# Kernel tuning notes

Measured on AMD Instinct MI355X. Metric: run time of the kernel, lower is better.

Reference implementation:

```python
import jax, jax.numpy as jnp
import numpy as np

D_MODEL = 2048
N_Q = 32
N_KV = 8  # num_heads // 4
HEAD_DIM = D_MODEL // N_Q  # 64
CTX = 2048


def precompute_rope_freqs(head_dim, max_seq_len):
    theta = 1.0 / (10000.0 ** (jnp.arange(0, head_dim, 2, dtype=jnp.float32) / head_dim))
    positions = jnp.arange(max_seq_len, dtype=jnp.float32)
    return jnp.outer(positions, theta)  # [T, head_dim//2]


def apply_rope(x, freqs):
    # x: [B, T, H, D]; freqs: [T, D//2]
    T = x.shape[1]
    f = freqs[:T][None, :, None, :]  # [1, T, 1, D//2]
    cos, sin = jnp.cos(f), jnp.sin(f)
    D = x.shape[-1]
    x1, x2 = x[..., : D // 2], x[..., D // 2 :]
    return jnp.concatenate([x1 * cos - x2 * sin, x1 * sin + x2 * cos], axis=-1)


def setup_inputs() -> dict:
    key = jax.random.key(0)
    ks = jax.random.split(key, 10)
    s = 0.02
    B, T = 1, CTX
    inp = {
        "x": jax.random.normal(ks[0], (B, T, D_MODEL), dtype=jnp.float32),
        "Wq": jax.random.normal(ks[1], (D_MODEL, N_Q * HEAD_DIM), dtype=jnp.float32) * s,
        "bq": jnp.zeros((N_Q * HEAD_DIM,), dtype=jnp.float32),
        "Wk": jax.random.normal(ks[2], (D_MODEL, N_KV * HEAD_DIM), dtype=jnp.float32) * s,
        "bk": jnp.zeros((N_KV * HEAD_DIM,), dtype=jnp.float32),
        "Wv": jax.random.normal(ks[3], (D_MODEL, N_KV * HEAD_DIM), dtype=jnp.float32) * s,
        "bv": jnp.zeros((N_KV * HEAD_DIM,), dtype=jnp.float32),
        "Wo": jax.random.normal(ks[4], (D_MODEL, D_MODEL), dtype=jnp.float32) * s,
        "bo": jnp.zeros((D_MODEL,), dtype=jnp.float32),
        "freqs": precompute_rope_freqs(HEAD_DIM, CTX),
    }
    return inp


def reference(x, Wq, bq, Wk, bk, Wv, bv, Wo, bo, freqs):
    B, T, C = x.shape
    q = (x @ Wq + bq).reshape(B, T, N_Q, HEAD_DIM)
    k = (x @ Wk + bk).reshape(B, T, N_KV, HEAD_DIM)
    v = (x @ Wv + bv).reshape(B, T, N_KV, HEAD_DIM)
    q = apply_rope(q, freqs)
    k = apply_rope(k, freqs)
    repeat = N_Q // N_KV
    # repeat_interleave along head dim: q head h uses kv head h // repeat
    k = jnp.repeat(k, repeat, axis=2)
    v = jnp.repeat(v, repeat, axis=2)
    # [B, H, T, D]
    q = q.transpose(0, 2, 1, 3)
    k = k.transpose(0, 2, 1, 3)
    v = v.transpose(0, 2, 1, 3)
    scale = 1.0 / jnp.sqrt(jnp.asarray(HEAD_DIM, dtype=x.dtype))
    scores = jnp.einsum("bhtd,bhsd->bhts", q, k) * scale  # [B, H, T, T]
    causal = jnp.tril(jnp.ones((T, T), dtype=bool))
    scores = jnp.where(causal[None, None], scores, jnp.finfo(scores.dtype).min)
    attn = jax.nn.softmax(scores, axis=-1)
    out = jnp.einsum("bhts,bhsd->bhtd", attn, v)  # [B, H, T, D]
    out = out.transpose(0, 2, 1, 3).reshape(B, T, C)
    return out @ Wo + bo
```

## Files before the change

### kernel.cpp

```cpp
#include <hip/hip_runtime.h>
#include <hip/hip_bf16.h>
#include <math.h>

#define T_CTX 2048
#define DM    2048
#define NQ    32
#define NKV   8
#define HD    64
#define QKV_LD 3072

typedef __attribute__((ext_vector_type(8))) short short8;
typedef __attribute__((ext_vector_type(4))) float floatx4;

__device__ __forceinline__ void gload_lds16(const void* g, void* l) {
  __builtin_amdgcn_global_load_lds(
      (const __attribute__((address_space(1))) void*)g,
      (__attribute__((address_space(3))) void*)l, 16, 0, 0);
}

__device__ __forceinline__ void tcast_body(const float* __restrict__ src,
                                           __hip_bfloat16* __restrict__ dst,
                                           int Ncols, int Krows, int bx, int by,
                                           int tid, float (*tile)[66]) {
  const int n0 = bx * 64, k0 = by * 64;
  const int c = tid & 63, r0 = tid >> 6;
#pragma unroll
  for (int s = 0; s < 16; ++s) {
    int r = r0 + 4 * s;
    tile[r][c] = src[(size_t)(k0 + r) * Ncols + n0 + c];
  }
  __syncthreads();
#pragma unroll
  for (int s = 0; s < 16; ++s) {
    int r = r0 + 4 * s;
    dst[(size_t)(n0 + r) * Krows + k0 + c] = __float2bfloat16(tile[c][r]);
  }
}

__global__ __launch_bounds__(256) void prep_kernel(
    const float* __restrict__ x, const float* __restrict__ Wq,
    const float* __restrict__ Wk, const float* __restrict__ Wv,
    const float* __restrict__ Wo, const float* __restrict__ bq,
    const float* __restrict__ bk, const float* __restrict__ bv,
    __hip_bfloat16* __restrict__ xb, __hip_bfloat16* __restrict__ wt,
    __hip_bfloat16* __restrict__ wot, float* __restrict__ bcat) {
  __shared__ float tile[64][66];
  const int bid = blockIdx.x;
  const int tid = threadIdx.x;
  if (bid < 2048) {
    const int i = bid * 256 + tid;
    const float4 a = ((const float4*)x)[2 * i];
    const float4 b = ((const float4*)x)[2 * i + 1];
    union { ushort u[8]; short8 v; } o;
    __hip_bfloat16 h;
    h = __float2bfloat16(a.x); o.u[0] = *(ushort*)&h;
    h = __float2bfloat16(a.y); o.u[1] = *(ushort*)&h;
    h = __float2bfloat16(a.z); o.u[2] = *(ushort*)&h;
    h = __float2bfloat16(a.w); o.u[3] = *(ushort*)&h;
    h = __float2bfloat16(b.x); o.u[4] = *(ushort*)&h;
    h = __float2bfloat16(b.y); o.u[5] = *(ushort*)&h;
    h = __float2bfloat16(b.z); o.u[6] = *(ushort*)&h;
    h = __float2bfloat16(b.w); o.u[7] = *(ushort*)&h;
    ((short8*)xb)[i] = o.v;
  } else if (bid < 3072) {
    const int lid = bid - 2048;
    tcast_body(Wq, wt, 2048, 2048, lid & 31, lid >> 5, tid, tile);
  } else if (bid < 3328) {
    const int lid = bid - 3072;
    tcast_body(Wk, wt + (size_t)2048 * 2048, 512, 2048, lid & 7, lid >> 3, tid, tile);
  } else if (bid < 3584) {
    const int lid = bid - 3328;
    tcast_body(Wv, wt + (size_t)2560 * 2048, 512, 2048, lid & 7, lid >> 3, tid, tile);
  } else if (bid < 4608) {
    const int lid = bid - 3584;
    tcast_body(Wo, wot, 2048, 2048, lid & 31, lid >> 5, tid, tile);
  } else {
    for (int i = tid; i < 3072; i += 256)
      bcat[i] = (i < 2048) ? bq[i] : ((i < 2560) ? bk[i - 2048] : bv[i - 2560]);
  }
}

template <typename OutT>
__global__ __launch_bounds__(256) void gemm_mfma_bt(
    const __hip_bfloat16* __restrict__ A, const __hip_bfloat16* __restrict__ Bt,
    const float* __restrict__ bias, OutT* __restrict__ C, int K, int ldc) {
  __shared__ alignas(16) short As[2][128 * 64];
  __shared__ alignas(16) short Bs[2][128 * 64];
  const int tid = threadIdx.x;
  const int lane = tid & 63;
  const int w = tid >> 6;
  const int wr = w >> 1, wc = w & 1;
  const int bm = blockIdx.y * 128, bn = blockIdx.x * 128;

  floatx4 acc[4][4];
#pragma unroll
  for (int m = 0; m < 4; ++m)
#pragma unroll
    for (int n = 0; n < 4; ++n) acc[m][n] = floatx4{0.f, 0.f, 0.f, 0.f};

  const int frag_kb = (lane >> 4) * 16;
  const int srow8 = lane >> 3;
  const int sbyte = (lane & 7) * 16;

  auto stage = [&](int buf, int k0) {
#pragma unroll
    for (int i = 0; i < 4; ++i) {
      const int r = w * 32 + i * 8 + srow8;
      const int gcb = sbyte ^ ((r & 7) << 4);
      gload_lds16((const char*)(A + (size_t)(bm + r) * K + k0) + gcb,
                  (char*)(As[buf]) + (w * 32 + i * 8) * 128);
      gload_lds16((const char*)(Bt + (size_t)(bn + r) * K + k0) + gcb,
                  (char*)(Bs[buf]) + (w * 32 + i * 8) * 128);
    }
  };

  stage(0, 0);
  __syncthreads();
  int cur = 0;
  for (int k0 = 0; k0 < K; k0 += 64) {
    if (k0 + 64 < K) stage(cur ^ 1, k0 + 64);
#pragma unroll
    for (int h = 0; h < 2; ++h) {
      short8 af[4], bf[4];
      const int kb = h * 64 + frag_kb;
#pragma unroll
      for (int m = 0; m < 4; ++m) {
        const int ar = wr * 64 + m * 16 + (lane & 15);
        af[m] = *(const short8*)((const char*)(As[cur]) + ar * 128 + (kb ^ ((ar & 7) << 4)));
      }
#pragma unroll
      for (int n = 0; n < 4; ++n) {
        const int br = wc * 64 + n * 16 + (lane & 15);
        bf[n] = *(const short8*)((const char*)(Bs[cur]) + br * 128 + (kb ^ ((br & 7) << 4)));
      }
#pragma unroll
      for (int m = 0; m < 4; ++m)
#pragma unroll
        for (int n = 0; n < 4; ++n)
          acc[m][n] = __builtin_amdgcn_mfma_f32_16x16x32_bf16(af[m], bf[n], acc[m][n], 0, 0, 0);
    }
    __syncthreads();
    cur ^= 1;
  }

  const int col_l = lane & 15;
  const int row_l = (lane >> 4) * 4;
#pragma unroll
  for (int n = 0; n < 4; ++n) {
    const int col = bn + wc * 64 + n * 16 + col_l;
    const float bv = bias[col];
#pragma unroll
    for (int m = 0; m < 4; ++m) {
      const int row0 = bm + wr * 64 + m * 16 + row_l;
#pragma unroll
      for (int r2 = 0; r2 < 4; ++r2) {
        const float v = acc[m][n][r2] + bv;
        if constexpr (sizeof(OutT) == 2)
          C[(size_t)(row0 + r2) * ldc + col] = __float2bfloat16(v);
        else
          C[(size_t)(row0 + r2) * ldc + col] = v;
      }
    }
  }
}

__global__ __launch_bounds__(256) void rope_kernel(__hip_bfloat16* __restrict__ qkv,
                                                   const float* __restrict__ freqs) {
  const int idx = blockIdx.x * 256 + threadIdx.x;
  const int i = idx & 31;
  const int h = (idx >> 5) % 40;
  const int t = idx / (40 * 32);
  const int base = (h < 32) ? h * HD : DM + (h - 32) * HD;
  __hip_bfloat16* p = qkv + (size_t)t * QKV_LD + base;
  const float f = freqs[t * 32 + i];
  float s, c;
  sincosf(f, &s, &c);
  const float x1 = __bfloat162float(p[i]);
  const float x2 = __bfloat162float(p[i + 32]);
  float r1 = x1 * c - x2 * s;
  float r2 = x1 * s + x2 * c;
  if (h < 32) { r1 *= 0.125f; r2 *= 0.125f; }
  p[i]      = __float2bfloat16(r1);
  p[i + 32] = __float2bfloat16(r2);
}

__global__ __launch_bounds__(256) void transpose_v_kernel(
    const __hip_bfloat16* __restrict__ qkv, __hip_bfloat16* __restrict__ vt) {
  __shared__ short tile[64][66];
  const int c0 = blockIdx.x * 64;
  const int t0 = blockIdx.y * 64;
  const int c = threadIdx.x & 63;
  const int r0 = threadIdx.x >> 6;
#pragma unroll
  for (int s = 0; s < 16; ++s) {
    int r = r0 + 4 * s;
    tile[r][c] = *(const short*)(qkv + (size_t)(t0 + r) * QKV_LD + DM + NKV * HD + c0 + c);
  }
  __syncthreads();
#pragma unroll
  for (int s = 0; s < 16; ++s) {
    int r = r0 + 4 * s;
    *(short*)(vt + (size_t)(c0 + r) * T_CTX + t0 + c) = tile[c][r];
  }
}

__global__ __launch_bounds__(256) void attn_mfma_kernel(
    const __hip_bfloat16* __restrict__ qkv, const __hip_bfloat16* __restrict__ vtg,
    __hip_bfloat16* __restrict__ O, __hip_bfloat16* __restrict__ Opart,
    float* __restrict__ mlpart) {
  const int bid = blockIdx.x;
  const int hp = bid / 48;
  const int w48 = bid % 48;
  int qb, t0, t1, half;
  bool split;
  if (w48 < 32) {
    qb = 31 - (w48 >> 1);
    half = w48 & 1;
    const int h = (qb + 2) >> 1;
    split = true;
    t0 = half ? h : 0;
    t1 = half ? (qb + 1) : h;
  } else {
    qb = 15 - (w48 - 32);
    half = 0; split = false;
    t0 = 0; t1 = qb + 1;
  }
  const int h0 = hp * 2;
  const int kvh = h0 >> 2;
  const int tid = threadIdx.x;
  const int lane = tid & 63;
  const int w = tid >> 6;
  const int l15 = lane & 15;
  const int lg = lane >> 4;
  const int qbase = qb * 64 + w * 16;

  __shared__ alignas(16) char Ks[64 * 128];
  __shared__ alignas(16) char Vts[64 * 128];
  __shared__ alignas(16) char Ps[4][2][16 * 128];

  short8 qf[2][2];
#pragma unroll
  for (int hh = 0; hh < 2; ++hh)
#pragma unroll
    for (int kh = 0; kh < 2; ++kh)
      qf[hh][kh] = *(const short8*)(qkv + (size_t)(qbase + l15) * QKV_LD +
                                    (h0 + hh) * HD + kh * 32 + lg * 8);

  floatx4 o_acc[2][4];
  float mrow[2][4], lrow[2][4];
#pragma unroll
  for (int hh = 0; hh < 2; ++hh)
#pragma unroll
    for (int n = 0; n < 4; ++n) o_acc[hh][n] = floatx4{0.f, 0.f, 0.f, 0.f};
#pragma unroll
  for (int hh = 0; hh < 2; ++hh)
#pragma unroll
    for (int r = 0; r < 4; ++r) { mrow[hh][r] = -INFINITY; lrow[hh][r] = 0.f; }

  const __hip_bfloat16* Kg = qkv + DM + kvh * HD;
  const int srow8 = lane >> 3;
  const int sbyte = (lane & 7) * 16;

  for (int kt = t0; kt < t1; ++kt) {
    const int s0 = kt * 64;
    __syncthreads();
#pragma unroll
    for (int i = 0; i < 2; ++i) {
      const int r = w * 16 + i * 8 + srow8;
      const int gcb = sbyte ^ ((r & 7) << 4);
      gload_lds16((const char*)(Kg + (size_t)(s0 + r) * QKV_LD) + gcb,
                  Ks + (w * 16 + i * 8) * 128);
      gload_lds16((const char*)(vtg + (size_t)(kvh * 64 + r) * T_CTX + s0) + gcb,
                  Vts + (w * 16 + i * 8) * 128);
    }
    __syncthreads();

    if (s0 > qbase + 15) continue;

    floatx4 sacc[2][4];
#pragma unroll
    for (int hh = 0; hh < 2; ++hh)
#pragma unroll
      for (int n = 0; n < 4; ++n) sacc[hh][n] = floatx4{0.f, 0.f, 0.f, 0.f};
#pragma unroll
    for (int kh = 0; kh < 2; ++kh) {
      short8 bf[4];
#pragma unroll
      for (int n = 0; n < 4; ++n) {
        const int kr = n * 16 + l15;
        bf[n] = *(const short8*)(Ks + kr * 128 + ((kh * 64 + lg * 16) ^ ((kr & 7) << 4)));
      }
#pragma unroll
      for (int hh = 0; hh < 2; ++hh)
#pragma unroll
        for (int n = 0; n < 4; ++n)
          sacc[hh][n] = __builtin_amdgcn_mfma_f32_16x16x32_bf16(qf[hh][kh], bf[n], sacc[hh][n], 0, 0, 0);
    }
    if (s0 + 63 > qbase) {
#pragma unroll
      for (int n = 0; n < 4; ++n)
#pragma unroll
        for (int r = 0; r < 4; ++r)
          if (s0 + n * 16 + l15 > qbase + lg * 4 + r) {
            sacc[0][n][r] = -INFINITY;
            sacc[1][n][r] = -INFINITY;
          }
    }
#pragma unroll
    for (int hh = 0; hh < 2; ++hh) {
#pragma unroll
      for (int r = 0; r < 4; ++r) {
        float t = fmaxf(fmaxf(sacc[hh][0][r], sacc[hh][1][r]),
                        fmaxf(sacc[hh][2][r], sacc[hh][3][r]));
        t = fmaxf(t, __shfl_xor(t, 1));
        t = fmaxf(t, __shfl_xor(t, 2));
        t = fmaxf(t, __shfl_xor(t, 4));
        t = fmaxf(t, __shfl_xor(t, 8));
        float mn = mrow[hh][r];
        if (t > mn + 8.f) {
          const float corr = __expf(mn - t);
          lrow[hh][r] *= corr;
#pragma unroll
          for (int n = 0; n < 4; ++n) o_acc[hh][n][r] *= corr;
          mn = t;
          mrow[hh][r] = t;
        }
        float pv[4];
        float ls = 0.f;
#pragma unroll
        for (int n = 0; n < 4; ++n) {
          pv[n] = __expf(sacc[hh][n][r] - mn);
          ls += pv[n];
        }
        ls += __shfl_xor(ls, 1);
        ls += __shfl_xor(ls, 2);
        ls += __shfl_xor(ls, 4);
        ls += __shfl_xor(ls, 8);
        lrow[hh][r] += ls;
        const int prow = lg * 4 + r;
#pragma unroll
        for (int n = 0; n < 4; ++n)
          *(__hip_bfloat16*)(Ps[w][hh] + prow * 128 +
                             (((n * 16 + l15) * 2) ^ ((prow & 7) << 4))) =
              __float2bfloat16(pv[n]);
      }
    }
#pragma unroll
    for (int kh = 0; kh < 2; ++kh) {
      short8 vf[4];
#pragma unroll
      for (int n = 0; n < 4; ++n) {
        const int vr = n * 16 + l15;
        vf[n] = *(const short8*)(Vts + vr * 128 + ((kh * 64 + lg * 16) ^ ((vr & 7) << 4)));
      }
#pragma unroll
      for (int hh = 0; hh < 2; ++hh) {
        const short8 pf = *(const short8*)(Ps[w][hh] + l15 * 128 +
                                           ((kh * 64 + lg * 16) ^ ((l15 & 7) << 4)));
#pragma unroll
        for (int n = 0; n < 4; ++n)
          o_acc[hh][n] = __builtin_amdgcn_mfma_f32_16x16x32_bf16(pf, vf[n], o_acc[hh][n], 0, 0, 0);
      }
    }
  }

  if (!split) {
#pragma unroll
    for (int hh = 0; hh < 2; ++hh) {
      float inv[4];
#pragma unroll
      for (int r = 0; r < 4; ++r) inv[r] = 1.f / lrow[hh][r];
#pragma unroll
      for (int n = 0; n < 4; ++n)
#pragma unroll
        for (int r = 0; r < 4; ++r)
          O[(size_t)(qbase + lg * 4 + r) * DM + (h0 + hh) * HD + n * 16 + l15] =
              __float2bfloat16(o_acc[hh][n][r] * inv[r]);
    }
  } else {
#pragma unroll
    for (int hh = 0; hh < 2; ++hh) {
      const int u = (((h0 + hh) << 4) + (qb - 16)) * 2 + half;
#pragma unroll
      for (int n = 0; n < 4; ++n)
#pragma unroll
        for (int r = 0; r < 4; ++r)
          Opart[(size_t)u * 4096 + (w * 16 + lg * 4 + r) * 64 + n * 16 + l15] =
              __float2bfloat16(o_acc[hh][n][r]);
      if (l15 == 0) {
#pragma unroll
        for (int r = 0; r < 4; ++r) {
          mlpart[u * 128 + w * 16 + lg * 4 + r]      = mrow[hh][r];
          mlpart[u * 128 + 64 + w * 16 + lg * 4 + r] = lrow[hh][r];
        }
      }
    }
  }
}

__global__ __launch_bounds__(256) void combine_kernel(
    const __hip_bfloat16* __restrict__ Opart, const float* __restrict__ mlpart,
    __hip_bfloat16* __restrict__ O) {
  const int head = blockIdx.x >> 4;
  const int sqb = blockIdx.x & 15;
  const int tid = threadIdx.x;
  const int r = tid >> 2;
  const int c0 = (tid & 3) * 16;
  const int u0 = (((head << 4) + sqb) << 1);
  const float m0 = mlpart[u0 * 128 + r];
  const float l0 = mlpart[u0 * 128 + 64 + r];
  const float m1 = mlpart[(u0 + 1) * 128 + r];
  const float l1 = mlpart[(u0 + 1) * 128 + 64 + r];
  const float M = fmaxf(m0, m1);
  const float a0 = __expf(m0 - M), a1 = __expf(m1 - M);
  const float inv = 1.f / (a0 * l0 + a1 * l1);
  const __hip_bfloat16* p0 = Opart + (size_t)u0 * 4096 + r * 64 + c0;
  const __hip_bfloat16* p1 = Opart + (size_t)(u0 + 1) * 4096 + r * 64 + c0;
  __hip_bfloat16* op = O + (size_t)((16 + sqb) * 64 + r) * DM + head * HD + c0;
#pragma unroll
  for (int j = 0; j < 16; ++j)
    op[j] = __float2bfloat16(
        (a0 * __bfloat162float(p0[j]) + a1 * __bfloat162float(p1[j])) * inv);
}

extern "C" void kernel_launch(void* const* d_in, const int* in_sizes, int n_in,
                              void* d_out, int out_size, void* d_ws, size_t ws_size,
                              hipStream_t stream) {
  const float* x     = (const float*)d_in[0];
  const float* Wq    = (const float*)d_in[1];
  const float* bq    = (const float*)d_in[2];
  const float* Wk    = (const float*)d_in[3];
  const float* bk    = (const float*)d_in[4];
  const float* Wv    = (const float*)d_in[5];
  const float* bv    = (const float*)d_in[6];
  const float* Wo    = (const float*)d_in[7];
  const float* bo    = (const float*)d_in[8];
  const float* freqs = (const float*)d_in[9];
  float* out = (float*)d_out;

  char* ws = (char*)d_ws;
  __hip_bfloat16* qkv   = (__hip_bfloat16*)ws;
  __hip_bfloat16* wt    = (__hip_bfloat16*)(ws + 12582912);
  __hip_bfloat16* obuf  = wt;
  __hip_bfloat16* xb    = (__hip_bfloat16*)(ws + 25165824);
  __hip_bfloat16* opart = xb;
  __hip_bfloat16* wot   = (__hip_bfloat16*)(ws + 33554432);
  __hip_bfloat16* vt    = (__hip_bfloat16*)(ws + 41943040);
  float*          bcat  = (float*)(ws + 44040192);
  float*          ml    = (float*)(ws + 44052480);

  const dim3 blk(256);

  prep_kernel<<<dim3(4609), blk, 0, stream>>>(x, Wq, Wk, Wv, Wo, bq, bk, bv,
                                              xb, wt, wot, bcat);

  gemm_mfma_bt<__hip_bfloat16><<<dim3(3072 / 128, 2048 / 128), blk, 0, stream>>>(
      xb, wt, bcat, qkv, DM, QKV_LD);

  rope_kernel<<<(T_CTX * 40 * 32) / 256, blk, 0, stream>>>(qkv, freqs);

  transpose_v_kernel<<<dim3(8, 32), blk, 0, stream>>>(qkv, vt);

  attn_mfma_kernel<<<dim3(16 * 48), blk, 0, stream>>>(qkv, vt, obuf, opart, ml);
  combine_kernel<<<dim3(512), blk, 0, stream>>>(opart, ml, obuf);

  gemm_mfma_bt<float><<<dim3(2048 / 128, 2048 / 128), blk, 0, stream>>>(
      obuf, wot, bo, out, DM, DM);
}
```

Measured before the change: 302.0 us.

## Double-buffer K/V tiles and transpose score MFMA for per-lane softmax rows

Adds two LDS buffers for K and V so the next tile's global-to-LDS load is issued before computing on the current tile, removing one barrier per iteration. It also swaps the MFMA operands so each lane holds a single query row, which cuts the row-max and row-sum shuffles and lets P be written as packed 4-element stores. The rescale decision becomes wave-uniform via __any, and MFMA blocks are wrapped in s_setprio. The costs are double the K/V LDS footprint and extra shuffles to broadcast the correction factor and the final row sums.

```diff
diff --git a/kernel.cpp b/kernel.cpp
--- a/kernel.cpp
+++ b/kernel.cpp
@@ -10,6 +10,7 @@
 #define QKV_LD 3072
 
 typedef __attribute__((ext_vector_type(8))) short short8;
+typedef __attribute__((ext_vector_type(4))) short short4v;
 typedef __attribute__((ext_vector_type(4))) float floatx4;
 
 __device__ __forceinline__ void gload_lds16(const void* g, void* l) {
@@ -234,8 +235,8 @@
   const int lg = lane >> 4;
   const int qbase = qb * 64 + w * 16;
 
-  __shared__ alignas(16) char Ks[64 * 128];
-  __shared__ alignas(16) char Vts[64 * 128];
+  __shared__ alignas(16) char Ks[2][64 * 128];
+  __shared__ alignas(16) char Vts[2][64 * 128];
   __shared__ alignas(16) char Ps[4][2][16 * 128];
 
   short8 qf[2][2];
@@ -247,121 +248,145 @@
                                     (h0 + hh) * HD + kh * 32 + lg * 8);
 
   floatx4 o_acc[2][4];
-  float mrow[2][4], lrow[2][4];
-#pragma unroll
-  for (int hh = 0; hh < 2; ++hh)
+  float mrow[2], lrow[2];
+#pragma unroll
+  for (int hh = 0; hh < 2; ++hh) {
 #pragma unroll
     for (int n = 0; n < 4; ++n) o_acc[hh][n] = floatx4{0.f, 0.f, 0.f, 0.f};
-#pragma unroll
-  for (int hh = 0; hh < 2; ++hh)
-#pragma unroll
-    for (int r = 0; r < 4; ++r) { mrow[hh][r] = -INFINITY; lrow[hh][r] = 0.f; }
+    mrow[hh] = -INFINITY;
+    lrow[hh] = 0.f;
+  }
 
   const __hip_bfloat16* Kg = qkv + DM + kvh * HD;
   const int srow8 = lane >> 3;
   const int sbyte = (lane & 7) * 16;
 
-  for (int kt = t0; kt < t1; ++kt) {
+  auto stage = [&](int buf, int kt) {
     const int s0 = kt * 64;
-    __syncthreads();
 #pragma unroll
     for (int i = 0; i < 2; ++i) {
       const int r = w * 16 + i * 8 + srow8;
       const int gcb = sbyte ^ ((r & 7) << 4);
       gload_lds16((const char*)(Kg + (size_t)(s0 + r) * QKV_LD) + gcb,
-                  Ks + (w * 16 + i * 8) * 128);
+                  Ks[buf] + (w * 16 + i * 8) * 128);
       gload_lds16((const char*)(vtg + (size_t)(kvh * 64 + r) * T_CTX + s0) + gcb,
-                  Vts + (w * 16 + i * 8) * 128);
+                  Vts[buf] + (w * 16 + i * 8) * 128);
+    }
+  };
+
+  stage(0, t0);
+  __syncthreads();
+  int cur = 0;
+
+  for (int kt = t0; kt < t1; ++kt) {
+    if (kt + 1 < t1) stage(cur ^ 1, kt + 1);
+    const int s0 = kt * 64;
+    if (s0 <= qbase + 15) {
+      floatx4 sacc[2][4];
+#pragma unroll
+      for (int hh = 0; hh < 2; ++hh)
+#pragma unroll
+        for (int n = 0; n < 4; ++n) sacc[hh][n] = floatx4{0.f, 0.f, 0.f, 0.f};
+#pragma unroll
+      for (int kh = 0; kh < 2; ++kh) {
+        short8 bf[4];
+#pragma unroll
+        for (int n = 0; n < 4; ++n) {
+          const int kr = n * 16 + l15;
+          bf[n] = *(const short8*)(Ks[cur] + kr * 128 + ((kh * 64 + lg * 16) ^ ((kr & 7) << 4)));
+        }
+        __builtin_amdgcn_s_setprio(1);
+#pragma unroll
+        for (int hh = 0; hh < 2; ++hh)
+#pragma unroll
+          for (int n = 0; n < 4; ++n)
+            sacc[hh][n] = __builtin_amdgcn_mfma_f32_16x16x32_bf16(bf[n], qf[hh][kh], sacc[hh][n], 0, 0, 0);
+        __builtin_amdgcn_s_setprio(0);
+      }
+      if (s0 + 63 > qbase) {
+#pragma unroll
+        for (int n = 0; n < 4; ++n)
+#pragma unroll
+          for (int r = 0; r < 4; ++r)
+            if (s0 + n * 16 + lg * 4 + r > qbase + l15) {
+              sacc[0][n][r] = -INFINITY;
+              sacc[1][n][r] = -INFINITY;
+            }
+      }
+#pragma unroll
+      for (int hh = 0; hh < 2; ++hh) {
+        float t01 = fmaxf(fmaxf(sacc[hh][0][0], sacc[hh][0][1]),
+                          fmaxf(sacc[hh][0][2], sacc[hh][0][3]));
+        float t23 = fmaxf(fmaxf(sacc[hh][1][0], sacc[hh][1][1]),
+                          fmaxf(sacc[hh][1][2], sacc[hh][1][3]));
+        float t45 = fmaxf(fmaxf(sacc[hh][2][0], sacc[hh][2][1]),
+                          fmaxf(sacc[hh][2][2], sacc[hh][2][3]));
+        float t67 = fmaxf(fmaxf(sacc[hh][3][0], sacc[hh][3][1]),
+                          fmaxf(sacc[hh][3][2], sacc[hh][3][3]));
+        float tmax = fmaxf(fmaxf(t01, t23), fmaxf(t45, t67));
+        tmax = fmaxf(tmax, __shfl_xor(tmax, 16));
+        tmax = fmaxf(tmax, __shfl_xor(tmax, 32));
+        float mn = mrow[hh];
+        if (__any(tmax > mn + 8.f)) {
+          const float mnew = fmaxf(mn, tmax);
+          const float corr = __expf(mn - mnew);
+          lrow[hh] *= corr;
+          float cb[4];
+#pragma unroll
+          for (int r = 0; r < 4; ++r) cb[r] = __shfl(corr, lg * 4 + r);
+#pragma unroll
+          for (int n = 0; n < 4; ++n)
+#pragma unroll
+            for (int r = 0; r < 4; ++r) o_acc[hh][n][r] *= cb[r];
+          mrow[hh] = mnew;
+          mn = mnew;
+        }
+        float ls = 0.f;
+        float pv[4][4];
+#pragma unroll
+        for (int n = 0; n < 4; ++n)
+#pragma unroll
+          for (int r = 0; r < 4; ++r) {
+            pv[n][r] = __expf(sacc[hh][n][r] - mn);
+            ls += pv[n][r];
+          }
+        ls += __shfl_xor(ls, 16);
+        ls += __shfl_xor(ls, 32);
+        lrow[hh] += ls;
+#pragma unroll
+        for (int n = 0; n < 4; ++n) {
+          short4v pk;
+#pragma unroll
+          for (int r = 0; r < 4; ++r) {
+            __hip_bfloat16 hb = __float2bfloat16(pv[n][r]);
+            pk[r] = *(short*)&hb;
+          }
+          *(short4v*)(Ps[w][hh] + l15 * 128 +
+                      (((n * 16 + lg * 4) * 2) ^ ((l15 & 7) << 4))) = pk;
+        }
+      }
+#pragma unroll
+      for (int kh = 0; kh < 2; ++kh) {
+        short8 vf[4];
+#pragma unroll
+        for (int n = 0; n < 4; ++n) {
+          const int vr = n * 16 + l15;
+          vf[n] = *(const short8*)(Vts[cur] + vr * 128 + ((kh * 64 + lg * 16) ^ ((vr & 7) << 4)));
+        }
+        __builtin_amdgcn_s_setprio(1);
+#pragma unroll
+        for (int hh = 0; hh < 2; ++hh) {
+          const short8 pf = *(const short8*)(Ps[w][hh] + l15 * 128 +
+                                             ((kh * 64 + lg * 16) ^ ((l15 & 7) << 4)));
+#pragma unroll
+          for (int n = 0; n < 4; ++n)
+            o_acc[hh][n] = __builtin_amdgcn_mfma_f32_16x16x32_bf16(pf, vf[n], o_acc[hh][n], 0, 0, 0);
+        }
+        __builtin_amdgcn_s_setprio(0);
+      }
     }
     __syncthreads();
-
-    if (s0 > qbase + 15) continue;
-
-    floatx4 sacc[2][4];
-#pragma unroll
-    for (int hh = 0; hh < 2; ++hh)
-#pragma unroll
-      for (int n = 0; n < 4; ++n) sacc[hh][n] = floatx4{0.f, 0.f, 0.f, 0.f};
-#pragma unroll
-    for (int kh = 0; kh < 2; ++kh) {
-      short8 bf[4];
-#pragma unroll
-      for (int n = 0; n < 4; ++n) {
-        const int kr = n * 16 + l15;
-        bf[n] = *(const short8*)(Ks + kr * 128 + ((kh * 64 + lg * 16) ^ ((kr & 7) << 4)));
-      }
-#pragma unroll
-      for (int hh = 0; hh < 2; ++hh)
-#pragma unroll
-        for (int n = 0; n < 4; ++n)
-          sacc[hh][n] = __builtin_amdgcn_mfma_f32_16x16x32_bf16(qf[hh][kh], bf[n], sacc[hh][n], 0, 0, 0);
-    }
-    if (s0 + 63 > qbase) {
-#pragma unroll
-      for (int n = 0; n < 4; ++n)
-#pragma unroll
-        for (int r = 0; r < 4; ++r)
-          if (s0 + n * 16 + l15 > qbase + lg * 4 + r) {
-            sacc[0][n][r] = -INFINITY;
-            sacc[1][n][r] = -INFINITY;
-          }
-    }
-#pragma unroll
-    for (int hh = 0; hh < 2; ++hh) {
-#pragma unroll
-      for (int r = 0; r < 4; ++r) {
-        float t = fmaxf(fmaxf(sacc[hh][0][r], sacc[hh][1][r]),
-                        fmaxf(sacc[hh][2][r], sacc[hh][3][r]));
-        t = fmaxf(t, __shfl_xor(t, 1));
-        t = fmaxf(t, __shfl_xor(t, 2));
-        t = fmaxf(t, __shfl_xor(t, 4));
-        t = fmaxf(t, __shfl_xor(t, 8));
-        float mn = mrow[hh][r];
-        if (t > mn + 8.f) {
-          const float corr = __expf(mn - t);
-          lrow[hh][r] *= corr;
-#pragma unroll
-          for (int n = 0; n < 4; ++n) o_acc[hh][n][r] *= corr;
-          mn = t;
-          mrow[hh][r] = t;
-        }
-        float pv[4];
-        float ls = 0.f;
-#pragma unroll
-        for (int n = 0; n < 4; ++n) {
-          pv[n] = __expf(sacc[hh][n][r] - mn);
-          ls += pv[n];
-        }
-        ls += __shfl_xor(ls, 1);
-        ls += __shfl_xor(ls, 2);
-        ls += __shfl_xor(ls, 4);
-        ls += __shfl_xor(ls, 8);
-        lrow[hh][r] += ls;
-        const int prow = lg * 4 + r;
-#pragma unroll
-        for (int n = 0; n < 4; ++n)
-          *(__hip_bfloat16*)(Ps[w][hh] + prow * 128 +
-                             (((n * 16 + l15) * 2) ^ ((prow & 7) << 4))) =
-              __float2bfloat16(pv[n]);
-      }
-    }
-#pragma unroll
-    for (int kh = 0; kh < 2; ++kh) {
-      short8 vf[4];
-#pragma unroll
-      for (int n = 0; n < 4; ++n) {
-        const int vr = n * 16 + l15;
-        vf[n] = *(const short8*)(Vts + vr * 128 + ((kh * 64 + lg * 16) ^ ((vr & 7) << 4)));
-      }
-#pragma unroll
-      for (int hh = 0; hh < 2; ++hh) {
-        const short8 pf = *(const short8*)(Ps[w][hh] + l15 * 128 +
-                                           ((kh * 64 + lg * 16) ^ ((l15 & 7) << 4)));
-#pragma unroll
-        for (int n = 0; n < 4; ++n)
-          o_acc[hh][n] = __builtin_amdgcn_mfma_f32_16x16x32_bf16(pf, vf[n], o_acc[hh][n], 0, 0, 0);
-      }
-    }
+    cur ^= 1;
   }
 
   if (!split) {
@@ -369,7 +394,7 @@
     for (int hh = 0; hh < 2; ++hh) {
       float inv[4];
 #pragma unroll
-      for (int r = 0; r < 4; ++r) inv[r] = 1.f / lrow[hh][r];
+      for (int r = 0; r < 4; ++r) inv[r] = 1.f / __shfl(lrow[hh], lg * 4 + r);
 #pragma unroll
       for (int n = 0; n < 4; ++n)
 #pragma unroll
@@ -387,12 +412,9 @@
         for (int r = 0; r < 4; ++r)
           Opart[(size_t)u * 4096 + (w * 16 + lg * 4 + r) * 64 + n * 16 + l15] =
               __float2bfloat16(o_acc[hh][n][r]);
-      if (l15 == 0) {
-#pragma unroll
-        for (int r = 0; r < 4; ++r) {
-          mlpart[u * 128 + w * 16 + lg * 4 + r]      = mrow[hh][r];
-          mlpart[u * 128 + 64 + w * 16 + lg * 4 + r] = lrow[hh][r];
-        }
+      if (lane < 16) {
+        mlpart[u * 128 + w * 16 + l15]      = mrow[hh];
+        mlpart[u * 128 + 64 + w * 16 + l15] = lrow[hh];
       }
     }
   }
```

New measurement: 267.8 us. 1.13x faster.
